# Performance work log

Measured on AMD Instinct MI355X. Metric: run time of the kernel, lower is better.

Reference implementation:

```python
import jax, jax.numpy as jnp
import numpy as np

EMBED = 512
HEADS = 8
QKV = 64
HEAD_DIM = QKV // HEADS  # 8


def setup_inputs() -> dict:
    key = jax.random.key(0)
    ks = jax.random.split(key, 10)
    B, S = 8, 2048
    s = 1.0 / np.sqrt(EMBED)
    inp = {
        "x": jax.random.normal(ks[0], (B, S, EMBED), dtype=jnp.float32),
        "mask_matrix": jnp.zeros((S, S), dtype=jnp.float32),
        "Wq": jax.random.uniform(ks[1], (EMBED, QKV), jnp.float32, -s, s),
        "bq": jax.random.uniform(ks[2], (QKV,), jnp.float32, -s, s),
        "Wk": jax.random.uniform(ks[3], (EMBED, QKV), jnp.float32, -s, s),
        "bk": jax.random.uniform(ks[4], (QKV,), jnp.float32, -s, s),
        "Wv": jax.random.uniform(ks[5], (EMBED, QKV), jnp.float32, -s, s),
        "bv": jax.random.uniform(ks[6], (QKV,), jnp.float32, -s, s),
        "Wu": jax.random.uniform(ks[7], (QKV, EMBED), jnp.float32, -1.0 / 8.0, 1.0 / 8.0),
        "bu": jax.random.uniform(ks[8], (EMBED,), jnp.float32, -1.0 / 8.0, 1.0 / 8.0),
    }
    return inp


def reference(x, mask_matrix, Wq, bq, Wk, bk, Wv, bv, Wu, bu):
    B, S, _ = x.shape
    # projections to fixed 64-dim
    Q = x @ Wq + bq  # [B,S,64]
    K = x @ Wk + bk
    V = x @ Wv + bv
    # faithful reshape (NO head transpose, matching the original view chain)
    Q = Q.reshape(B * HEADS, S, HEAD_DIM)
    K = K.reshape(B * HEADS, S, HEAD_DIM)
    V = V.reshape(B * HEADS, S, HEAD_DIM)
    scores = jnp.einsum('gqd,gkd->gqk', Q, K)  # [B*H,S,S]
    scores = (scores + mask_matrix[None, :, :]) / np.sqrt(HEAD_DIM)
    probs = jax.nn.softmax(scores, axis=2)
    attn = jnp.einsum('gqk,gkd->gqd', probs, V)  # [B*H,S,hd]
    attn = attn.reshape(B, S, HEADS * HEAD_DIM)
    return attn @ Wu + bu
```

## Files before the change

kernel.cpp:

```cpp
#include <hip/hip_runtime.h>

typedef float f32x4 __attribute__((ext_vector_type(4)));
typedef float f32x16 __attribute__((ext_vector_type(16)));
typedef short s16x8 __attribute__((ext_vector_type(8)));
typedef unsigned int u32x2 __attribute__((ext_vector_type(2)));
typedef unsigned int u32x4 __attribute__((ext_vector_type(4)));

#define DEVFN static __device__ __forceinline__

constexpr int S_ = 2048;
constexpr int E_ = 512;
constexpr int D_ = 8;
constexpr int P_ = 64;
constexpr float C2 = 0.35355339059327373f * 1.4426950408889634f;


constexpr size_t FLAG_OFF = 0;
constexpr size_t WT_OFF   = 256;
constexpr size_t WUT_OFF  = WT_OFF  + (size_t)192 * 512 * 2;
constexpr size_t ATT_OFF  = WUT_OFF + (size_t)512 * 64 * 2;
constexpr size_t QG_O  = 0;
constexpr size_t KG_O  = (size_t)64 * 2048 * 8 * 2;
constexpr size_t VTG_O = KG_O * 2;

DEVFN short f2bf(float f) {
  unsigned u = __builtin_bit_cast(unsigned, f);
  return (short)((u + 0x7FFFu + ((u >> 16) & 1u)) >> 16);
}

DEVFN unsigned pkbf(float lo, float hi) {
  unsigned r;
  asm("v_cvt_pk_bf16_f32 %0, %1, %2" : "=v"(r) : "v"(lo), "v"(hi));
  return r;
}

DEVFN float fexp2(float x) {
#if __has_builtin(__builtin_amdgcn_exp2f)
  return __builtin_amdgcn_exp2f(x);
#else
  return exp2f(x);
#endif
}

DEVFN f32x16 mfma32(s16x8 a, s16x8 b, f32x16 c) {
  return __builtin_amdgcn_mfma_f32_32x32x16_bf16(a, b, c, 0, 0, 0);
}

DEVFN f32x16 zero16() {
  f32x16 z = {0,0,0,0,0,0,0,0,0,0,0,0,0,0,0,0};
  return z;
}

__global__ __launch_bounds__(256)
void prep_kernel(const float* __restrict__ Wq, const float* __restrict__ Wk,
                 const float* __restrict__ Wv, const float* __restrict__ Wu,
                 const float* __restrict__ maskm, short* __restrict__ WT,
                 short* __restrict__ WUT, int* __restrict__ flag)
{
  int bid = blockIdx.x, tid = threadIdx.x;
  if (bid < 48) {
    int base = (bid * 256 + tid) * 8;
#pragma unroll
    for (int j = 0; j < 8; ++j) {
      int idx = base + j;
      int n = idx >> 9, k = idx & 511;
      const float* W = (n < 64) ? Wq : ((n < 128) ? Wk : Wv);
      WT[idx] = f2bf(W[k * 64 + (n & 63)]);
    }
  } else if (bid < 56) {
    int base = ((bid - 48) * 256 + tid) * 16;
#pragma unroll
    for (int j = 0; j < 16; ++j) {
      int idx = base + j;
      int n = idx >> 6, k = idx & 63;
      WUT[idx] = f2bf(Wu[k * 512 + n]);
    }
  } else {
    const f32x4* m4 = (const f32x4*)maskm;
    int base = (bid - 56) * 4096;
    unsigned any = 0;
#pragma unroll
    for (int i = 0; i < 16; ++i) {
      f32x4 v = m4[base + i * 256 + tid];
      any |= __builtin_bit_cast(unsigned, v[0]) | __builtin_bit_cast(unsigned, v[1])
           | __builtin_bit_cast(unsigned, v[2]) | __builtin_bit_cast(unsigned, v[3]);
    }
    if (any != 0) atomicOr(flag, 1);
  }
}

__global__ __launch_bounds__(384)
void proj_kernel(const float* __restrict__ x, const short* __restrict__ WT,
                 const float* __restrict__ bq, const float* __restrict__ bk,
                 const float* __restrict__ bv, short* __restrict__ QG,
                 short* __restrict__ KG, short* __restrict__ VTG)
{
  __shared__ short xl[32 * 520];
  int tid = threadIdx.x;
  int mb = blockIdx.x * 32;
  for (int i = tid; i < 32 * 128; i += 384) {
    int row = i >> 7, c4 = i & 127;
    f32x4 v = *(const f32x4*)(x + (size_t)(mb + row) * E_ + c4 * 4);
    u32x2 w;
    w[0] = pkbf(v[0], v[1]);
    w[1] = pkbf(v[2], v[3]);
    *(u32x2*)(&xl[row * 520 + c4 * 4]) = w;
  }
  __syncthreads();
  int lane = tid & 63, wvi = tid >> 6;
  int l31 = lane & 31, h = lane >> 5;
  int nstrip = wvi * 32;
  f32x16 acc = zero16();
#pragma unroll 4
  for (int kk = 0; kk < E_; kk += 16) {
    s16x8 af = *(const s16x8*)(WT + (size_t)(nstrip + l31) * E_ + kk + 8 * h);
    s16x8 bf = *(const s16x8*)(&xl[l31 * 520 + kk + 8 * h]);
    acc = mfma32(af, bf, acc);
  }
  int token = mb + l31;
  int bidx = token >> 11, s = token & 2047;
  int gg = bidx * 8 + (s >> 8);
#pragma unroll
  for (int i = 0; i < 4; ++i) {
    int n0 = nstrip + 8 * i + 4 * h;
    int proj = n0 >> 6;
    int wi = n0 & 63;
    int head = wi >> 3, db = wi & 7;
    const float* bias = (proj == 0) ? bq : ((proj == 1) ? bk : bv);
    float sc = (proj == 0) ? C2 : 1.0f;
    float f0 = (acc[4*i+0] + bias[wi+0]) * sc;
    float f1 = (acc[4*i+1] + bias[wi+1]) * sc;
    float f2 = (acc[4*i+2] + bias[wi+2]) * sc;
    float f3 = (acc[4*i+3] + bias[wi+3]) * sc;
    int p = ((s & 255) << 3) + head;
    if (proj == 2) {
      int k16 = p & 15;
      int slot = (k16 & 3) + ((k16 >> 2) & 1) * 8 + (k16 >> 3) * 4;
      size_t vb = (size_t)gg * (S_ * D_) + (size_t)(p >> 4) * 128 + slot;
      VTG[vb + (db+0)*16] = f2bf(f0);
      VTG[vb + (db+1)*16] = f2bf(f1);
      VTG[vb + (db+2)*16] = f2bf(f2);
      VTG[vb + (db+3)*16] = f2bf(f3);
    } else {
      short* dst = (proj == 0) ? QG : KG;
      u32x2 o;
      o[0] = pkbf(f0, f1);
      o[1] = pkbf(f2, f3);
      *(u32x2*)(dst + ((size_t)gg * S_ + p) * D_ + db) = o;
    }
  }
}

__global__ __launch_bounds__(512, 4)
void attn_kernel(const short* __restrict__ QG, const short* __restrict__ KG,
                 const short* __restrict__ VTG, const float* __restrict__ maskm,
                 const int* __restrict__ flag, short* __restrict__ ATT)
{
  __shared__ short K_lds[S_ * D_];
  __shared__ short V_lds[128 * 9 * 16];
  __shared__ short Z_lds[8];
  int bid = blockIdx.x;
  int swz = (bid & 7) * 64 + (bid >> 3);
  int g  = swz >> 3;
  int qb = (swz & 7) * 256;
  int tid = threadIdx.x;
  {
    const u32x4* ks = (const u32x4*)(KG  + (size_t)g * (S_ * D_));
    const u32x4* vs = (const u32x4*)(VTG + (size_t)g * (S_ * D_));
    u32x4* kd = (u32x4*)K_lds;
#pragma unroll
    for (int it = 0; it < 4; ++it) {
      int i = tid + it * 512;
      kd[i] = ks[i];
      u32x4 v = vs[i];
      int t = i >> 4, rem = i & 15;
      *(u32x4*)(&V_lds[t * 144 + rem * 8]) = v;
    }
    if (tid < 8) Z_lds[tid] = 0;
    unsigned one2 = 0x3F803F80u;
    u32x2 o2; o2[0] = one2; o2[1] = one2;
    int t = tid >> 2, qr = tid & 3;
    *(u32x2*)(&V_lds[t * 144 + 128 + qr * 4]) = o2;
  }
  __syncthreads();

  int lane = tid & 63, wvi = tid >> 6;
  int l31 = lane & 31, h = lane >> 5;
  int q = qb + wvi * 32 + l31;
  bool hi = (h != 0);
  int dcl = (l31 < 8) ? l31 : 8;
  s16x8 zero8 = {0,0,0,0,0,0,0,0};

  s16x8 qf = hi ? zero8
                : *(const s16x8*)(QG + ((size_t)g * S_ + q) * D_);
  const short* kptr = hi ? Z_lds : &K_lds[l31 * 8];
  int kstride = hi ? 0 : 32 * 8;
  const short* vptr = &V_lds[dcl * 16 + 8 * h];
  f32x16 acc = zero16();
  bool usemask = (*flag != 0);

  for (int kb = 0; kb < S_; kb += 32) {
    s16x8 kf = *(const s16x8*)kptr;
    kptr += kstride;
    f32x16 st = mfma32(kf, qf, zero16());
    s16x8 va1 = *(const s16x8*)vptr;
    s16x8 va2 = *(const s16x8*)(vptr + 144);
    vptr += 288;
    float p[16];
    if (!usemask) {
#pragma unroll
      for (int r = 0; r < 16; ++r) p[r] = fexp2(st[r]);
    } else {
#pragma unroll
      for (int r = 0; r < 16; ++r) {
        int key = kb + (r & 3) + 8 * (r >> 2) + 4 * h;
        p[r] = fexp2(st[r] + maskm[(size_t)q * S_ + key] * C2);
      }
    }
    u32x4 b1, b2;
    b1[0] = pkbf(p[0],  p[1]);
    b1[1] = pkbf(p[2],  p[3]);
    b1[2] = pkbf(p[4],  p[5]);
    b1[3] = pkbf(p[6],  p[7]);
    b2[0] = pkbf(p[8],  p[9]);
    b2[1] = pkbf(p[10], p[11]);
    b2[2] = pkbf(p[12], p[13]);
    b2[3] = pkbf(p[14], p[15]);
    acc = mfma32(va1, __builtin_bit_cast(s16x8, b1), acc);
    acc = mfma32(va2, __builtin_bit_cast(s16x8, b2), acc);
  }
  float d0 = acc[4];
  float dp = __shfl_xor(d0, 32, 64);
  float den = hi ? dp : d0;
  float inv = __builtin_amdgcn_rcpf(den);
  u32x2 o;
  o[0] = pkbf(acc[0] * inv, acc[1] * inv);
  o[1] = pkbf(acc[2] * inv, acc[3] * inv);
  size_t token = (size_t)(g >> 3) * S_ + (g & 7) * 256 + (q >> 3);
  int cbase = (q & 7) * 8 + 4 * h;
  *(u32x2*)(ATT + token * P_ + cbase) = o;
}

__global__ __launch_bounds__(256)
void out_kernel(const short* __restrict__ ATT, const short* __restrict__ WUT,
                const float* __restrict__ bu, float* __restrict__ out)
{
  int tid = threadIdx.x;
  int lane = tid & 63, wvi = tid >> 6;
  int l31 = lane & 31, h = lane >> 5;
  int mb = blockIdx.x * 32;
  int nb = wvi * 128;
  f32x16 acc[4];
#pragma unroll
  for (int nf = 0; nf < 4; ++nf) acc[nf] = zero16();
#pragma unroll
  for (int kk = 0; kk < 64; kk += 16) {
    s16x8 af = *(const s16x8*)(ATT + (size_t)(mb + l31) * P_ + kk + 8 * h);
#pragma unroll
    for (int nf = 0; nf < 4; ++nf) {
      s16x8 bf = *(const s16x8*)(WUT + (size_t)(nb + nf * 32 + l31) * P_ + kk + 8 * h);
      acc[nf] = mfma32(af, bf, acc[nf]);
    }
  }
#pragma unroll
  for (int nf = 0; nf < 4; ++nf) {
    int n = nb + nf * 32 + l31;
    float bias = bu[n];
#pragma unroll
    for (int r = 0; r < 16; ++r) {
      int m = (r & 3) + 8 * (r >> 2) + 4 * h;
      out[(size_t)(mb + m) * E_ + n] = acc[nf][r] + bias;
    }
  }
}

extern "C" void kernel_launch(void* const* d_in, const int* in_sizes, int n_in,
                              void* d_out, int out_size, void* d_ws, size_t ws_size,
                              hipStream_t stream) {
  const float* x     = (const float*)d_in[0];
  const float* maskm = (const float*)d_in[1];
  const float* Wq    = (const float*)d_in[2];
  const float* bq    = (const float*)d_in[3];
  const float* Wk    = (const float*)d_in[4];
  const float* bk    = (const float*)d_in[5];
  const float* Wv    = (const float*)d_in[6];
  const float* bv    = (const float*)d_in[7];
  const float* Wu    = (const float*)d_in[8];
  const float* bu    = (const float*)d_in[9];
  float* out = (float*)d_out;
  char* ws = (char*)d_ws;
  char* ob = (char*)d_out;
  int*   flag = (int*)(ws + FLAG_OFF);
  short* WT   = (short*)(ws + WT_OFF);
  short* WUT  = (short*)(ws + WUT_OFF);
  short* ATT  = (short*)(ws + ATT_OFF);
  short* QG   = (short*)(ob + QG_O);
  short* KG   = (short*)(ob + KG_O);
  short* VTG  = (short*)(ob + VTG_O);

  hipMemsetAsync(flag, 0, 16, stream);
  prep_kernel<<<312, 256, 0, stream>>>(Wq, Wk, Wv, Wu, maskm, WT, WUT, flag);
  proj_kernel<<<512, 384, 0, stream>>>(x, WT, bq, bk, bv, QG, KG, VTG);
  attn_kernel<<<512, 512, 0, stream>>>(QG, KG, VTG, maskm, flag, ATT);
  out_kernel<<<512, 256, 0, stream>>>(ATT, WUT, bu, out);
}
```

Measured before the change: 76.51 us.

## Fuse output projection into attention kernel and drop flag memset

Fuses the output projection GEMM into the attention kernel: each block stages its 32 normalized attention tokens in LDS and multiplies them by the transposed Wu, writing the final output directly. This removes the separate out_kernel launch and the global round-trip of the attention intermediate. The mask-nonzero flag becomes a per-block array written unconditionally, so the hipMemsetAsync launch is dropped. The no-mask loop is also unrolled by two. The trade-off is more LDS and a longer tail per attention block.

```diff
diff --git a/kernel.cpp b/kernel.cpp
--- a/kernel.cpp
+++ b/kernel.cpp
@@ -15,13 +15,12 @@
 constexpr float C2 = 0.35355339059327373f * 1.4426950408889634f;
 
 
-constexpr size_t FLAG_OFF = 0;
-constexpr size_t WT_OFF   = 256;
-constexpr size_t WUT_OFF  = WT_OFF  + (size_t)192 * 512 * 2;
-constexpr size_t ATT_OFF  = WUT_OFF + (size_t)512 * 64 * 2;
-constexpr size_t QG_O  = 0;
-constexpr size_t KG_O  = (size_t)64 * 2048 * 8 * 2;
-constexpr size_t VTG_O = KG_O * 2;
+constexpr size_t FLAGA_OFF = 0;
+constexpr size_t WT_OFF    = 1024;
+constexpr size_t WUT_OFF   = WT_OFF + (size_t)192 * 512 * 2;
+constexpr size_t QG_OFF    = WUT_OFF + (size_t)512 * 64 * 2;
+constexpr size_t KG_OFF    = QG_OFF + (size_t)64 * 2048 * 8 * 2;
+constexpr size_t VTG_OFF   = KG_OFF + (size_t)64 * 2048 * 8 * 2;
 
 DEVFN short f2bf(float f) {
   unsigned u = __builtin_bit_cast(unsigned, f);
@@ -55,7 +54,7 @@
 void prep_kernel(const float* __restrict__ Wq, const float* __restrict__ Wk,
                  const float* __restrict__ Wv, const float* __restrict__ Wu,
                  const float* __restrict__ maskm, short* __restrict__ WT,
-                 short* __restrict__ WUT, int* __restrict__ flag)
+                 short* __restrict__ WUT, int* __restrict__ flagA)
 {
   int bid = blockIdx.x, tid = threadIdx.x;
   if (bid < 48) {
@@ -76,6 +75,9 @@
       WUT[idx] = f2bf(Wu[k * 512 + n]);
     }
   } else {
+    __shared__ int bf_;
+    if (tid == 0) bf_ = 0;
+    __syncthreads();
     const f32x4* m4 = (const f32x4*)maskm;
     int base = (bid - 56) * 4096;
     unsigned any = 0;
@@ -85,7 +87,9 @@
       any |= __builtin_bit_cast(unsigned, v[0]) | __builtin_bit_cast(unsigned, v[1])
            | __builtin_bit_cast(unsigned, v[2]) | __builtin_bit_cast(unsigned, v[3]);
     }
-    if (any != 0) atomicOr(flag, 1);
+    if (any != 0) atomicOr(&bf_, 1);
+    __syncthreads();
+    if (tid == 0) flagA[bid - 56] = bf_;
   }
 }
 
@@ -151,14 +155,43 @@
   }
 }
 
+#define ATTN_TILE(kb, USEMASK)                                          \
+  {                                                                     \
+    s16x8 kf = *(const s16x8*)kptr; kptr += kstride;                    \
+    f32x16 st = mfma32(kf, qf, zero16());                               \
+    s16x8 va1 = *(const s16x8*)vptr;                                    \
+    s16x8 va2 = *(const s16x8*)(vptr + 144);                            \
+    vptr += 288;                                                        \
+    float p[16];                                                        \
+    _Pragma("unroll")                                                   \
+    for (int r = 0; r < 16; ++r) {                                      \
+      float sv = st[r];                                                 \
+      if (USEMASK) {                                                    \
+        int key = (kb) + (r & 3) + 8 * (r >> 2) + 4 * h;                \
+        sv += maskm[(size_t)q * S_ + key] * C2;                         \
+      }                                                                 \
+      p[r] = fexp2(sv);                                                 \
+    }                                                                   \
+    u32x4 b1, b2;                                                       \
+    b1[0] = pkbf(p[0],  p[1]);  b1[1] = pkbf(p[2],  p[3]);              \
+    b1[2] = pkbf(p[4],  p[5]);  b1[3] = pkbf(p[6],  p[7]);              \
+    b2[0] = pkbf(p[8],  p[9]);  b2[1] = pkbf(p[10], p[11]);             \
+    b2[2] = pkbf(p[12], p[13]); b2[3] = pkbf(p[14], p[15]);             \
+    acc = mfma32(va1, __builtin_bit_cast(s16x8, b1), acc);              \
+    acc = mfma32(va2, __builtin_bit_cast(s16x8, b2), acc);              \
+  }
+
 __global__ __launch_bounds__(512, 4)
 void attn_kernel(const short* __restrict__ QG, const short* __restrict__ KG,
                  const short* __restrict__ VTG, const float* __restrict__ maskm,
-                 const int* __restrict__ flag, short* __restrict__ ATT)
+                 const int* __restrict__ flagA, const short* __restrict__ WUT,
+                 const float* __restrict__ bu, float* __restrict__ out)
 {
   __shared__ short K_lds[S_ * D_];
   __shared__ short V_lds[128 * 9 * 16];
+  __shared__ short A_lds[32 * 68];
   __shared__ short Z_lds[8];
+  __shared__ int   sm_flag;
   int bid = blockIdx.x;
   int swz = (bid & 7) * 64 + (bid >> 3);
   int g  = swz >> 3;
@@ -181,6 +214,13 @@
     u32x2 o2; o2[0] = one2; o2[1] = one2;
     int t = tid >> 2, qr = tid & 3;
     *(u32x2*)(&V_lds[t * 144 + 128 + qr * 4]) = o2;
+    if (tid < 64) {
+      const u32x4* fa4 = (const u32x4*)flagA;
+      u32x4 f = fa4[tid];
+      unsigned anyf = f[0] | f[1] | f[2] | f[3];
+      unsigned long long bb = __ballot(anyf != 0);
+      if (tid == 0) sm_flag = (bb != 0ull) ? 1 : 0;
+    }
   }
   __syncthreads();
 
@@ -197,37 +237,13 @@
   int kstride = hi ? 0 : 32 * 8;
   const short* vptr = &V_lds[dcl * 16 + 8 * h];
   f32x16 acc = zero16();
-  bool usemask = (*flag != 0);
-
-  for (int kb = 0; kb < S_; kb += 32) {
-    s16x8 kf = *(const s16x8*)kptr;
-    kptr += kstride;
-    f32x16 st = mfma32(kf, qf, zero16());
-    s16x8 va1 = *(const s16x8*)vptr;
-    s16x8 va2 = *(const s16x8*)(vptr + 144);
-    vptr += 288;
-    float p[16];
-    if (!usemask) {
-#pragma unroll
-      for (int r = 0; r < 16; ++r) p[r] = fexp2(st[r]);
-    } else {
-#pragma unroll
-      for (int r = 0; r < 16; ++r) {
-        int key = kb + (r & 3) + 8 * (r >> 2) + 4 * h;
-        p[r] = fexp2(st[r] + maskm[(size_t)q * S_ + key] * C2);
-      }
-    }
-    u32x4 b1, b2;
-    b1[0] = pkbf(p[0],  p[1]);
-    b1[1] = pkbf(p[2],  p[3]);
-    b1[2] = pkbf(p[4],  p[5]);
-    b1[3] = pkbf(p[6],  p[7]);
-    b2[0] = pkbf(p[8],  p[9]);
-    b2[1] = pkbf(p[10], p[11]);
-    b2[2] = pkbf(p[12], p[13]);
-    b2[3] = pkbf(p[14], p[15]);
-    acc = mfma32(va1, __builtin_bit_cast(s16x8, b1), acc);
-    acc = mfma32(va2, __builtin_bit_cast(s16x8, b2), acc);
+  bool usemask = (sm_flag != 0);
+
+  if (!usemask) {
+#pragma unroll 2
+    for (int kb = 0; kb < S_; kb += 32) ATTN_TILE(kb, false)
+  } else {
+    for (int kb = 0; kb < S_; kb += 32) ATTN_TILE(kb, true)
   }
   float d0 = acc[4];
   float dp = __shfl_xor(d0, 32, 64);
@@ -236,41 +252,29 @@
   u32x2 o;
   o[0] = pkbf(acc[0] * inv, acc[1] * inv);
   o[1] = pkbf(acc[2] * inv, acc[3] * inv);
-  size_t token = (size_t)(g >> 3) * S_ + (g & 7) * 256 + (q >> 3);
-  int cbase = (q & 7) * 8 + 4 * h;
-  *(u32x2*)(ATT + token * P_ + cbase) = o;
-}
-
-__global__ __launch_bounds__(256)
-void out_kernel(const short* __restrict__ ATT, const short* __restrict__ WUT,
-                const float* __restrict__ bu, float* __restrict__ out)
-{
-  int tid = threadIdx.x;
-  int lane = tid & 63, wvi = tid >> 6;
-  int l31 = lane & 31, h = lane >> 5;
-  int mb = blockIdx.x * 32;
-  int nb = wvi * 128;
-  f32x16 acc[4];
-#pragma unroll
-  for (int nf = 0; nf < 4; ++nf) acc[nf] = zero16();
+  int local = wvi * 4 + (l31 >> 3);
+  int col = (l31 & 7) * 8 + 4 * h;
+  *(u32x2*)(&A_lds[local * 68 + col]) = o;
+  __syncthreads();
+  int nb = wvi * 64;
+  f32x16 accA = zero16(), accB = zero16();
 #pragma unroll
   for (int kk = 0; kk < 64; kk += 16) {
-    s16x8 af = *(const s16x8*)(ATT + (size_t)(mb + l31) * P_ + kk + 8 * h);
-#pragma unroll
-    for (int nf = 0; nf < 4; ++nf) {
-      s16x8 bf = *(const s16x8*)(WUT + (size_t)(nb + nf * 32 + l31) * P_ + kk + 8 * h);
-      acc[nf] = mfma32(af, bf, acc[nf]);
-    }
-  }
-#pragma unroll
-  for (int nf = 0; nf < 4; ++nf) {
-    int n = nb + nf * 32 + l31;
-    float bias = bu[n];
-#pragma unroll
-    for (int r = 0; r < 16; ++r) {
-      int m = (r & 3) + 8 * (r >> 2) + 4 * h;
-      out[(size_t)(mb + m) * E_ + n] = acc[nf][r] + bias;
-    }
+    s16x8 af  = *(const s16x8*)(&A_lds[l31 * 68 + kk + 8 * h]);
+    s16x8 bfA = *(const s16x8*)(WUT + (size_t)(nb + l31) * P_ + kk + 8 * h);
+    s16x8 bfB = *(const s16x8*)(WUT + (size_t)(nb + 32 + l31) * P_ + kk + 8 * h);
+    accA = mfma32(af, bfA, accA);
+    accB = mfma32(af, bfB, accB);
+  }
+  size_t token_base = (size_t)(g >> 3) * S_ + (g & 7) * 256 + (qb >> 3);
+  size_t obase = token_base * E_;
+  int nA = nb + l31, nB = nb + 32 + l31;
+  float biasA = bu[nA], biasB = bu[nB];
+#pragma unroll
+  for (int r = 0; r < 16; ++r) {
+    int m = (r & 3) + 8 * (r >> 2) + 4 * h;
+    out[obase + (size_t)m * E_ + nA] = accA[r] + biasA;
+    out[obase + (size_t)m * E_ + nB] = accB[r] + biasB;
   }
 }
 
@@ -289,18 +293,14 @@
   const float* bu    = (const float*)d_in[9];
   float* out = (float*)d_out;
   char* ws = (char*)d_ws;
-  char* ob = (char*)d_out;
-  int*   flag = (int*)(ws + FLAG_OFF);
-  short* WT   = (short*)(ws + WT_OFF);
-  short* WUT  = (short*)(ws + WUT_OFF);
-  short* ATT  = (short*)(ws + ATT_OFF);
-  short* QG   = (short*)(ob + QG_O);
-  short* KG   = (short*)(ob + KG_O);
-  short* VTG  = (short*)(ob + VTG_O);
-
-  hipMemsetAsync(flag, 0, 16, stream);
-  prep_kernel<<<312, 256, 0, stream>>>(Wq, Wk, Wv, Wu, maskm, WT, WUT, flag);
+  int*   flagA = (int*)(ws + FLAGA_OFF);
+  short* WT    = (short*)(ws + WT_OFF);
+  short* WUT   = (short*)(ws + WUT_OFF);
+  short* QG    = (short*)(ws + QG_OFF);
+  short* KG    = (short*)(ws + KG_OFF);
+  short* VTG   = (short*)(ws + VTG_OFF);
+
+  prep_kernel<<<312, 256, 0, stream>>>(Wq, Wk, Wv, Wu, maskm, WT, WUT, flagA);
   proj_kernel<<<512, 384, 0, stream>>>(x, WT, bq, bk, bv, QG, KG, VTG);
-  attn_kernel<<<512, 512, 0, stream>>>(QG, KG, VTG, maskm, flag, ATT);
-  out_kernel<<<512, 256, 0, stream>>>(ATT, WUT, bu, out);
-}
+  attn_kernel<<<512, 512, 0, stream>>>(QG, KG, VTG, maskm, flagA, WUT, bu, out);
+}
```

After: 65.22 us. 14.7% less time.
